# Optimization experiments

Measured on AMD Instinct MI355X. Metric: run time of the kernel, lower is better.

## Reference

```python
import jax, jax.numpy as jnp
import numpy as np

DIM = 1024
H = 8
HK = DIM // H  # head key dim = 128 (expand_k=1.0)
HV = DIM // H  # head value dim = 128 (expand_v=1.0)
GLR = 16       # gate low-rank dim (fla default)
GATE_LOGIT_NORMALIZER = 16.0
EPS = 1e-5
B, T = 2, 512


def setup_inputs() -> dict:
    key = jax.random.key(0)
    ks = jax.random.split(key, 9)
    s = lambda k, shp: jax.random.normal(k, shp, jnp.float32) * (shp[0] ** -0.5)
    return {
        "x": jax.random.normal(ks[0], (B, T, DIM), jnp.float32),
        "Wq": s(ks[1], (DIM, DIM)),
        "Wk": s(ks[2], (DIM, DIM)),
        "Wv": s(ks[3], (DIM, DIM)),
        "Wg": s(ks[4], (DIM, DIM)),
        "Wgk1": s(ks[5], (DIM, GLR)),
        "Wgk2": s(ks[6], (GLR, DIM)),
        "bgk2": jnp.zeros((DIM,), jnp.float32),
        "g_norm_w": jnp.ones((HV,), jnp.float32),
        "Wo": s(ks[7], (DIM, DIM)),
    }


def _gla_forward(x, Wq, Wk, Wv, Wg, Wgk1, Wgk2, bgk2, g_norm_w, Wo):
    b, t, _ = x.shape
    # projections
    q = (x @ Wq).reshape(b, t, H, HK) * (HK ** -0.5)
    k = (x @ Wk).reshape(b, t, H, HK)
    v = (x @ Wv).reshape(b, t, H, HV)
    # low-rank forget gate: logsigmoid / normalizer, per key channel
    gk = (jax.nn.log_sigmoid((x @ Wgk1) @ Wgk2 + bgk2) / GATE_LOGIT_NORMALIZER)
    gk = gk.reshape(b, t, H, HK)

    # recurrent decay-gated linear attention:
    #   S_t = diag(exp(gk_t)) @ S_{t-1} + k_t^T v_t ; o_t = q_t @ S_t
    def step(h, inp):
        qt, kt, vt, gt = inp  # each [B, H, HK] / [B, H, HV]
        h = h * jnp.exp(gt)[..., None] + kt[..., None] * vt[..., None, :]
        ot = jnp.einsum("bhk,bhkv->bhv", qt, h)
        return h, ot

    h0 = jnp.zeros((b, H, HK, HV), x.dtype)
    xs = (
        q.transpose(1, 0, 2, 3),
        k.transpose(1, 0, 2, 3),
        v.transpose(1, 0, 2, 3),
        gk.transpose(1, 0, 2, 3),
    )
    _, o = jax.lax.scan(step, h0, xs)  # o: [T, B, H, HV]
    o = o.transpose(1, 0, 2, 3)        # [B, T, H, HV]

    # gated RMSNorm with swish gate over per-head value dim, then output proj
    g = (x @ Wg).reshape(b, t, H, HV)
    rms = jax.lax.rsqrt(jnp.mean(o * o, axis=-1, keepdims=True) + EPS)
    o = (o * rms) * g_norm_w * (g * jax.nn.sigmoid(g))
    return o.reshape(b, t, DIM) @ Wo


def reference(x, Wq, Wk, Wv, Wg, Wgk1, Wgk2, bgk2, g_norm_w, Wo):
    return _gla_forward(x, Wq, Wk, Wv, Wg, Wgk1, Wgk2, bgk2, g_norm_w, Wo)
```

## Files before the change

kernel.cpp:

```cpp
#include <hip/hip_runtime.h>
#include <hip/hip_bf16.h>
#include <math.h>

#define BT     1024
#define NH     8
#define SEGLEN 32
#define NSEG   16
#define NBH    16
#define QKS    136
#define VTS    40
#define AMS    40

typedef __attribute__((ext_vector_type(8))) short short8;
typedef __attribute__((ext_vector_type(4))) short sh4;
typedef __attribute__((ext_vector_type(4))) float f32x4;

__device__ __forceinline__ float bitf(short u) {
    union { float f; unsigned i; } x; x.i = ((unsigned)(unsigned short)u) << 16; return x.f;
}
__device__ __forceinline__ short f2bf(float f) {
    union { float f; unsigned u; } x; x.f = f;
    unsigned r = x.u + 0x7FFF + ((x.u >> 16) & 1);
    return (short)(r >> 16);
}
__device__ __forceinline__ void gload_lds16(const short* g, short* l) {
    __builtin_amdgcn_global_load_lds(
        (const __attribute__((address_space(1))) unsigned int*)g,
        (__attribute__((address_space(3))) unsigned int*)l, 16, 0, 0);
}

__global__ __launch_bounds__(256) void cast_all(
    const float* __restrict__ Wq, const float* __restrict__ Wk,
    const float* __restrict__ Wv, const float* __restrict__ Wg,
    const float* __restrict__ Wo, const float* __restrict__ X,
    short* __restrict__ WT, short* __restrict__ Xb)
{
    const int z = blockIdx.z;
    const int tid = threadIdx.x;
    if (z == 5) {
        const int id = blockIdx.y * 32 + blockIdx.x;
        const int i = id * 1024 + tid * 4;
        float4 a = *(const float4*)(X + i);
        sh4 v;
        v[0] = f2bf(a.x); v[1] = f2bf(a.y); v[2] = f2bf(a.z); v[3] = f2bf(a.w);
        *(sh4*)(Xb + i) = v;
        return;
    }
    const float* W = (z == 0) ? Wq : (z == 1) ? Wk : (z == 2) ? Wv : (z == 3) ? Wg : Wo;
    short* T = WT + (size_t)z * (1u << 20);
    __shared__ float tile[32][33];
    const int k0 = blockIdx.y * 32, n0 = blockIdx.x * 32;
    const int row = tid >> 3, c4 = (tid & 7) << 2;
    float4 f = *(const float4*)(W + (size_t)(k0 + row) * 1024 + n0 + c4);
    tile[row][c4 + 0] = f.x; tile[row][c4 + 1] = f.y;
    tile[row][c4 + 2] = f.z; tile[row][c4 + 3] = f.w;
    __syncthreads();
    short* o = T + (size_t)(n0 + row) * 1024 + k0 + c4;
    o[0] = f2bf(tile[c4 + 0][row]); o[1] = f2bf(tile[c4 + 1][row]);
    o[2] = f2bf(tile[c4 + 2][row]); o[3] = f2bf(tile[c4 + 3][row]);
}

__global__ __launch_bounds__(256) void proj_gemm(
    const short* __restrict__ Xb, const short* __restrict__ WT,
    short* __restrict__ QKVG)
{
    const int z = blockIdx.z;
    const float scale = (z == 0) ? 0.08838834764831845f : 1.0f;
    short* C = QKVG + (size_t)z * (1u << 20);
    const short* B = WT + (size_t)z * (1u << 20);

    __shared__ __align__(16) short As[8 * 64 * 8];
    __shared__ __align__(16) short Bs[8 * 128 * 8];
    const int tid = threadIdx.x;
    const int wave = tid >> 6, lane = tid & 63;
    const int wm = (wave >> 1) * 32, wn = (wave & 1) * 64;
    const int m15 = lane & 15, q = lane >> 4;
    const int m0 = blockIdx.y * 64, n0 = blockIdx.x * 128;

    f32x4 acc[2][4];
    #pragma unroll
    for (int i = 0; i < 2; i++)
        #pragma unroll
        for (int j = 0; j < 4; j++)
            acc[i][j] = (f32x4){0.f, 0.f, 0.f, 0.f};

    for (int kb0 = 0; kb0 < 1024; kb0 += 64) {
        __syncthreads();
        #pragma unroll
        for (int c = 0; c < 2; c++) {
            const int k8 = wave * 2 + c;
            gload_lds16(Xb + (size_t)(m0 + lane) * 1024 + kb0 + k8 * 8,
                        &As[(k8 * 64) * 8]);
            #pragma unroll
            for (int rh = 0; rh < 2; rh++)
                gload_lds16(B + (size_t)(n0 + rh * 64 + lane) * 1024 + kb0 + k8 * 8,
                            &Bs[(k8 * 128 + rh * 64) * 8]);
        }
        __syncthreads();
        #pragma unroll
        for (int s = 0; s < 2; s++) {
            const int k8 = s * 4 + q;
            short8 af[2], bf[4];
            #pragma unroll
            for (int i = 0; i < 2; i++)
                af[i] = *(const short8*)&As[(k8 * 64 + wm + i * 16 + m15) * 8];
            #pragma unroll
            for (int j = 0; j < 4; j++)
                bf[j] = *(const short8*)&Bs[(k8 * 128 + wn + j * 16 + m15) * 8];
            #pragma unroll
            for (int i = 0; i < 2; i++)
                #pragma unroll
                for (int j = 0; j < 4; j++)
                    acc[i][j] = __builtin_amdgcn_mfma_f32_16x16x32_bf16(af[i], bf[j], acc[i][j], 0, 0, 0);
        }
    }
    #pragma unroll
    for (int i = 0; i < 2; i++)
        #pragma unroll
        for (int j = 0; j < 4; j++)
            #pragma unroll
            for (int rr = 0; rr < 4; rr++)
                C[(size_t)(m0 + wm + i * 16 + q * 4 + rr) * 1024 + n0 + wn + j * 16 + m15] =
                    f2bf(acc[i][j][rr] * scale);
}

__global__ __launch_bounds__(256) void wo_gemm(
    const short* __restrict__ A, const short* __restrict__ B, float* __restrict__ C)
{
    __shared__ __align__(16) short As[8 * 64 * 8];
    __shared__ __align__(16) short Bs[8 * 64 * 8];
    const int tid = threadIdx.x;
    const int wave = tid >> 6, lane = tid & 63;
    const int wm = (wave >> 1) * 32, wn = (wave & 1) * 32;
    const int m15 = lane & 15, q = lane >> 4;
    const int m0 = blockIdx.y * 64, n0 = blockIdx.x * 64;

    f32x4 acc[2][2];
    #pragma unroll
    for (int i = 0; i < 2; i++)
        #pragma unroll
        for (int j = 0; j < 2; j++)
            acc[i][j] = (f32x4){0.f, 0.f, 0.f, 0.f};

    for (int kb0 = 0; kb0 < 1024; kb0 += 64) {
        __syncthreads();
        #pragma unroll
        for (int c = 0; c < 2; c++) {
            const int k8 = wave * 2 + c;
            gload_lds16(A + (size_t)(m0 + lane) * 1024 + kb0 + k8 * 8, &As[(k8 * 64) * 8]);
            gload_lds16(B + (size_t)(n0 + lane) * 1024 + kb0 + k8 * 8, &Bs[(k8 * 64) * 8]);
        }
        __syncthreads();
        #pragma unroll
        for (int s = 0; s < 2; s++) {
            const int k8 = s * 4 + q;
            short8 af[2], bf[2];
            #pragma unroll
            for (int i = 0; i < 2; i++)
                af[i] = *(const short8*)&As[(k8 * 64 + wm + i * 16 + m15) * 8];
            #pragma unroll
            for (int j = 0; j < 2; j++)
                bf[j] = *(const short8*)&Bs[(k8 * 64 + wn + j * 16 + m15) * 8];
            #pragma unroll
            for (int i = 0; i < 2; i++)
                #pragma unroll
                for (int j = 0; j < 2; j++)
                    acc[i][j] = __builtin_amdgcn_mfma_f32_16x16x32_bf16(af[i], bf[j], acc[i][j], 0, 0, 0);
        }
    }
    #pragma unroll
    for (int i = 0; i < 2; i++)
        #pragma unroll
        for (int j = 0; j < 2; j++)
            #pragma unroll
            for (int rr = 0; rr < 4; rr++)
                C[(size_t)(m0 + wm + i * 16 + q * 4 + rr) * 1024 + n0 + wn + j * 16 + m15] =
                    acc[i][j][rr];
}

__global__ __launch_bounds__(256) void gk_proj(
    const short* __restrict__ Xb, const float* __restrict__ Wgk1,
    const float* __restrict__ Wgk2, const float* __restrict__ bgk2,
    short* __restrict__ GK)
{
    const int row = blockIdx.x, tid = threadIdx.x;
    float p[16];
    #pragma unroll
    for (int j = 0; j < 16; j++) p[j] = 0.f;
    for (int d = tid; d < 1024; d += 256) {
        float xv = bitf(Xb[(size_t)row * 1024 + d]);
        #pragma unroll
        for (int j = 0; j < 16; j++)
            p[j] = fmaf(xv, Wgk1[d * 16 + j], p[j]);
    }
    #pragma unroll
    for (int j = 0; j < 16; j++)
        for (int off = 32; off; off >>= 1) p[j] += __shfl_down(p[j], off);
    __shared__ float zp[4][16];
    __shared__ float z[16];
    const int lane = tid & 63, w = tid >> 6;
    if (lane == 0) {
        #pragma unroll
        for (int j = 0; j < 16; j++) zp[w][j] = p[j];
    }
    __syncthreads();
    if (tid < 16) z[tid] = zp[0][tid] + zp[1][tid] + zp[2][tid] + zp[3][tid];
    __syncthreads();
    for (int c = tid; c < 1024; c += 256) {
        float acc = bgk2[c];
        #pragma unroll
        for (int j = 0; j < 16; j++)
            acc = fmaf(z[j], Wgk2[j * 1024 + c], acc);
        float ls = fminf(acc, 0.f) - log1pf(expf(-fabsf(acc)));
        GK[(size_t)row * 1024 + c] = f2bf(ls * (1.f / 16.f));
    }
}

__global__ __launch_bounds__(256) void scan_chunk(
    const short* __restrict__ Q, const short* __restrict__ K,
    const short* __restrict__ V, short* GKQT,
    float* __restrict__ O, short* __restrict__ SS, float* __restrict__ DSEG)
{
    const int seg = blockIdx.x;
    const int bh  = blockIdx.y;
    const int b = bh >> 3, h = bh & 7;
    const int tid = threadIdx.x;
    const size_t rowbase = (size_t)(b * 512 + seg * SEGLEN) * 1024 + h * 128;

    __shared__ __align__(16) short Qt[32 * QKS];
    __shared__ __align__(16) short Kt[32 * QKS];
    __shared__ __align__(16) short Vs[32 * 128];
    __shared__ __align__(16) short VT[128 * VTS];
    __shared__ __align__(16) short KhT[128 * VTS];
    __shared__ __align__(16) short Am[32 * AMS];

    if (tid < 128) {
        const int ch = tid;
        float gsum = 0.f;
        float ktf[32];
        #pragma unroll
        for (int t = 0; t < 32; t++) {
            const size_t a = rowbase + (size_t)t * 1024 + ch;
            float g  = bitf(GKQT[a]);
            float kv = bitf(K[a]);
            float qv = bitf(Q[a]);
            gsum += g;
            float eg  = expf(gsum);
            float emg = expf(-gsum);
            short qts = f2bf(qv * eg);
            Qt[t * QKS + ch] = qts;
            GKQT[a] = qts;
            float ktv = kv * emg;
            Kt[t * QKS + ch] = f2bf(ktv);
            ktf[t] = ktv;
        }
        float eGend = expf(gsum);
        DSEG[(bh * NSEG + seg) * 128 + ch] = eGend;
        #pragma unroll
        for (int t4 = 0; t4 < 8; t4++) {
            sh4 p;
            p[0] = f2bf(ktf[4 * t4 + 0] * eGend);
            p[1] = f2bf(ktf[4 * t4 + 1] * eGend);
            p[2] = f2bf(ktf[4 * t4 + 2] * eGend);
            p[3] = f2bf(ktf[4 * t4 + 3] * eGend);
            *(sh4*)&KhT[ch * VTS + 4 * t4] = p;
        }
    } else {
        const int u = tid - 128;
        #pragma unroll
        for (int i = 0; i < 4; i++) {
            const int idx = u + i * 128;
            const int t = idx >> 4, c = idx & 15;
            short8 vv = *(const short8*)&V[rowbase + (size_t)t * 1024 + c * 8];
            *(short8*)&Vs[t * 128 + c * 8] = vv;
        }
    }
    __syncthreads();
    {
        const int ch = tid >> 1, t0 = (tid & 1) * 16;
        #pragma unroll
        for (int j = 0; j < 4; j++) {
            sh4 p;
            p[0] = Vs[(t0 + 4 * j + 0) * 128 + ch];
            p[1] = Vs[(t0 + 4 * j + 1) * 128 + ch];
            p[2] = Vs[(t0 + 4 * j + 2) * 128 + ch];
            p[3] = Vs[(t0 + 4 * j + 3) * 128 + ch];
            *(sh4*)&VT[ch * VTS + t0 + 4 * j] = p;
        }
    }
    __syncthreads();

    const int wave = tid >> 6, lane = tid & 63;
    const int m15 = lane & 15, q = lane >> 4;

    {
        const int mi = wave >> 1, ni = wave & 1;
        f32x4 a1 = (f32x4){0.f, 0.f, 0.f, 0.f};
        #pragma unroll
        for (int kc = 0; kc < 4; kc++) {
            short8 af = *(const short8*)&Qt[(mi * 16 + m15) * QKS + kc * 32 + q * 8];
            short8 bf = *(const short8*)&Kt[(ni * 16 + m15) * QKS + kc * 32 + q * 8];
            a1 = __builtin_amdgcn_mfma_f32_16x16x32_bf16(af, bf, a1, 0, 0, 0);
        }
        #pragma unroll
        for (int rr = 0; rr < 4; rr++) {
            const int t = mi * 16 + q * 4 + rr, s = ni * 16 + m15;
            Am[t * AMS + s] = (t >= s) ? f2bf(a1[rr]) : (short)0;
        }
    }
    __syncthreads();

    {
        const int mi = wave >> 1, nb = (wave & 1) * 4;
        short8 af = *(const short8*)&Am[(mi * 16 + m15) * AMS + q * 8];
        #pragma unroll
        for (int jj = 0; jj < 4; jj++) {
            short8 bf = *(const short8*)&VT[((nb + jj) * 16 + m15) * VTS + q * 8];
            f32x4 a2 = (f32x4){0.f, 0.f, 0.f, 0.f};
            a2 = __builtin_amdgcn_mfma_f32_16x16x32_bf16(af, bf, a2, 0, 0, 0);
            #pragma unroll
            for (int rr = 0; rr < 4; rr++)
                O[rowbase + (size_t)(mi * 16 + q * 4 + rr) * 1024 + (nb + jj) * 16 + m15] = a2[rr];
        }
    }

    {
        const size_t sbase = (size_t)(bh * NSEG + seg) * 16384;
        #pragma unroll
        for (int m2 = 0; m2 < 2; m2++) {
            const int mrow = wave * 2 + m2;
            short8 af = *(const short8*)&KhT[(mrow * 16 + m15) * VTS + q * 8];
            #pragma unroll
            for (int ni = 0; ni < 8; ni++) {
                short8 bf = *(const short8*)&VT[(ni * 16 + m15) * VTS + q * 8];
                f32x4 a3 = (f32x4){0.f, 0.f, 0.f, 0.f};
                a3 = __builtin_amdgcn_mfma_f32_16x16x32_bf16(af, bf, a3, 0, 0, 0);
                #pragma unroll
                for (int rr = 0; rr < 4; rr++)
                    SS[sbase + (size_t)(mrow * 16 + q * 4 + rr) * 128 + ni * 16 + m15] =
                        f2bf(a3[rr]);
            }
        }
    }
}

__global__ __launch_bounds__(256) void stitch(
    short* __restrict__ SS, const float* __restrict__ DSEG)
{
    const int slice = blockIdx.x;
    const int bh = blockIdx.y, tid = threadIdx.x;
    __shared__ float dloc[NSEG][16];
    dloc[tid >> 4][tid & 15] = DSEG[(bh * NSEG + (tid >> 4)) * 128 + slice * 16 + (tid & 15)];
    __syncthreads();
    float run[8];
    #pragma unroll
    for (int j = 0; j < 8; j++) run[j] = 0.f;
    for (int seg = 0; seg < NSEG; seg++) {
        const size_t base = (size_t)(bh * NSEG + seg) * 16384 + slice * 2048;
        #pragma unroll
        for (int j = 0; j < 8; j++) {
            const int e = j * 256 + tid;
            float tmp = bitf(SS[base + e]);
            SS[base + e] = f2bf(run[j]);
            run[j] = fmaf(run[j], dloc[seg][(e >> 7)], tmp);
        }
    }
}

__global__ __launch_bounds__(256) void corr_gnorm(
    const short* __restrict__ QT, const short* __restrict__ SS,
    const float* __restrict__ O, const short* __restrict__ G,
    const float* __restrict__ gnw, short* __restrict__ Obf)
{
    const int seg = blockIdx.x;
    const int bh = blockIdx.y;
    const int b = bh >> 3, h = bh & 7;
    const int tid = threadIdx.x;
    __shared__ float qt[SEGLEN][128];
    __shared__ float red[4][16];
    const size_t rowbase = (size_t)(b * 512 + seg * SEGLEN) * 1024 + h * 128;
    {
        const int t = tid >> 3, c0 = (tid & 7) * 16;
        #pragma unroll
        for (int c = 0; c < 16; c++)
            qt[t][c0 + c] = bitf(QT[rowbase + (size_t)t * 1024 + c0 + c]);
    }
    __syncthreads();
    const size_t sbase = (size_t)(bh * NSEG + seg) * 16384;
    const int v = tid & 127, th = tid >> 7;
    float acc[16];
    #pragma unroll
    for (int tt = 0; tt < 16; tt++) acc[tt] = 0.f;
    for (int k = 0; k < 128; k++) {
        float sv = bitf(SS[sbase + (size_t)k * 128 + v]);
        #pragma unroll
        for (int tt = 0; tt < 16; tt++)
            acc[tt] = fmaf(qt[th * 16 + tt][k], sv, acc[tt]);
    }
    float o[16], ss[16];
    #pragma unroll
    for (int tt = 0; tt < 16; tt++) {
        const int t = th * 16 + tt;
        o[tt] = O[rowbase + (size_t)t * 1024 + v] + acc[tt];
        ss[tt] = o[tt] * o[tt];
    }
    #pragma unroll
    for (int tt = 0; tt < 16; tt++)
        #pragma unroll
        for (int off = 32; off; off >>= 1)
            ss[tt] += __shfl_xor(ss[tt], off);
    const int wv = tid >> 6;
    if ((tid & 63) == 0) {
        #pragma unroll
        for (int tt = 0; tt < 16; tt++) red[wv][tt] = ss[tt];
    }
    __syncthreads();
    const float gw = gnw[v];
    #pragma unroll
    for (int tt = 0; tt < 16; tt++) {
        const int t = th * 16 + tt;
        float ms = (red[th * 2][tt] + red[th * 2 + 1][tt]) * (1.f / 128.f);
        float r = rsqrtf(ms + 1e-5f);
        float g = bitf(G[rowbase + (size_t)t * 1024 + v]);
        float sg = g / (1.f + expf(-g));
        Obf[rowbase + (size_t)t * 1024 + v] = f2bf(o[tt] * r * gw * sg);
    }
}

extern "C" void kernel_launch(void* const* d_in, const int* in_sizes, int n_in,
                              void* d_out, int out_size, void* d_ws, size_t ws_size,
                              hipStream_t stream)
{
    const float* X    = (const float*)d_in[0];
    const float* Wq   = (const float*)d_in[1];
    const float* Wk   = (const float*)d_in[2];
    const float* Wv   = (const float*)d_in[3];
    const float* Wg   = (const float*)d_in[4];
    const float* Wgk1 = (const float*)d_in[5];
    const float* Wgk2 = (const float*)d_in[6];
    const float* bgk2 = (const float*)d_in[7];
    const float* gnw  = (const float*)d_in[8];
    const float* Wo   = (const float*)d_in[9];
    float* OUT = (float*)d_out;

    short* QKVG = (short*)d_ws;
    short* GK   = QKVG + (4u << 20);
    float* Ob   = (float*)(GK + (1u << 20));
    short* SS   = (short*)(Ob + (1u << 20));
    float* DS   = (float*)(SS + (4u << 20));
    short* WT   = (short*)(DS + 32768);
    short* Xb   = WT + (5u << 20);
    short* Obf  = QKVG;

    cast_all<<<dim3(32, 32, 6), 256, 0, stream>>>(Wq, Wk, Wv, Wg, Wo, X, WT, Xb);
    proj_gemm<<<dim3(8, 16, 4), 256, 0, stream>>>(Xb, WT, QKVG);
    gk_proj<<<dim3(BT), 256, 0, stream>>>(Xb, Wgk1, Wgk2, bgk2, GK);
    scan_chunk<<<dim3(NSEG, NBH), 256, 0, stream>>>(
        QKVG, QKVG + (1u << 20), QKVG + (2u << 20), GK, Ob, SS, DS);
    stitch<<<dim3(8, NBH), 256, 0, stream>>>(SS, DS);
    corr_gnorm<<<dim3(NSEG, NBH), 256, 0, stream>>>(
        GK, SS, Ob, QKVG + (3u << 20), gnw, Obf);
    wo_gemm<<<dim3(16, 16), 256, 0, stream>>>(Obf, WT + (4u << 20), OUT);
}
```

Measured before the change: 174.1 us.

## Use MFMA for inter-chunk correction, transpose state layout, shrink proj tiles

The chunk state in SS is now stored transposed (value-major), and the stitch kernel is changed to match, so each thread now uses a single per-key decay value. corr_gnorm replaces its scalar FMA loop over the 128-wide state with bf16 MFMA tiles loaded into LDS asynchronously, and does the RMS reduction with lane shuffles within 16-lane groups. proj_gemm tiles drop from 64x128 to 64x64 and the grid doubles, which gives more blocks and better occupancy but less reuse of each loaded tile.

```diff
diff --git a/kernel.cpp b/kernel.cpp
--- a/kernel.cpp
+++ b/kernel.cpp
@@ -70,18 +70,18 @@
     const short* B = WT + (size_t)z * (1u << 20);
 
     __shared__ __align__(16) short As[8 * 64 * 8];
-    __shared__ __align__(16) short Bs[8 * 128 * 8];
+    __shared__ __align__(16) short Bs[8 * 64 * 8];
     const int tid = threadIdx.x;
     const int wave = tid >> 6, lane = tid & 63;
-    const int wm = (wave >> 1) * 32, wn = (wave & 1) * 64;
+    const int wm = (wave >> 1) * 32, wn = (wave & 1) * 32;
     const int m15 = lane & 15, q = lane >> 4;
-    const int m0 = blockIdx.y * 64, n0 = blockIdx.x * 128;
-
-    f32x4 acc[2][4];
+    const int m0 = blockIdx.y * 64, n0 = blockIdx.x * 64;
+
+    f32x4 acc[2][2];
     #pragma unroll
     for (int i = 0; i < 2; i++)
         #pragma unroll
-        for (int j = 0; j < 4; j++)
+        for (int j = 0; j < 2; j++)
             acc[i][j] = (f32x4){0.f, 0.f, 0.f, 0.f};
 
     for (int kb0 = 0; kb0 < 1024; kb0 += 64) {
@@ -89,35 +89,31 @@
         #pragma unroll
         for (int c = 0; c < 2; c++) {
             const int k8 = wave * 2 + c;
-            gload_lds16(Xb + (size_t)(m0 + lane) * 1024 + kb0 + k8 * 8,
-                        &As[(k8 * 64) * 8]);
-            #pragma unroll
-            for (int rh = 0; rh < 2; rh++)
-                gload_lds16(B + (size_t)(n0 + rh * 64 + lane) * 1024 + kb0 + k8 * 8,
-                            &Bs[(k8 * 128 + rh * 64) * 8]);
+            gload_lds16(Xb + (size_t)(m0 + lane) * 1024 + kb0 + k8 * 8, &As[(k8 * 64) * 8]);
+            gload_lds16(B  + (size_t)(n0 + lane) * 1024 + kb0 + k8 * 8, &Bs[(k8 * 64) * 8]);
         }
         __syncthreads();
         #pragma unroll
         for (int s = 0; s < 2; s++) {
             const int k8 = s * 4 + q;
-            short8 af[2], bf[4];
+            short8 af[2], bf[2];
             #pragma unroll
             for (int i = 0; i < 2; i++)
                 af[i] = *(const short8*)&As[(k8 * 64 + wm + i * 16 + m15) * 8];
             #pragma unroll
-            for (int j = 0; j < 4; j++)
-                bf[j] = *(const short8*)&Bs[(k8 * 128 + wn + j * 16 + m15) * 8];
+            for (int j = 0; j < 2; j++)
+                bf[j] = *(const short8*)&Bs[(k8 * 64 + wn + j * 16 + m15) * 8];
             #pragma unroll
             for (int i = 0; i < 2; i++)
                 #pragma unroll
-                for (int j = 0; j < 4; j++)
+                for (int j = 0; j < 2; j++)
                     acc[i][j] = __builtin_amdgcn_mfma_f32_16x16x32_bf16(af[i], bf[j], acc[i][j], 0, 0, 0);
         }
     }
     #pragma unroll
     for (int i = 0; i < 2; i++)
         #pragma unroll
-        for (int j = 0; j < 4; j++)
+        for (int j = 0; j < 2; j++)
             #pragma unroll
             for (int rr = 0; rr < 4; rr++)
                 C[(size_t)(m0 + wm + i * 16 + q * 4 + rr) * 1024 + n0 + wn + j * 16 + m15] =
@@ -329,10 +325,10 @@
         #pragma unroll
         for (int m2 = 0; m2 < 2; m2++) {
             const int mrow = wave * 2 + m2;
-            short8 af = *(const short8*)&KhT[(mrow * 16 + m15) * VTS + q * 8];
+            short8 af = *(const short8*)&VT[(mrow * 16 + m15) * VTS + q * 8];
             #pragma unroll
             for (int ni = 0; ni < 8; ni++) {
-                short8 bf = *(const short8*)&VT[(ni * 16 + m15) * VTS + q * 8];
+                short8 bf = *(const short8*)&KhT[(ni * 16 + m15) * VTS + q * 8];
                 f32x4 a3 = (f32x4){0.f, 0.f, 0.f, 0.f};
                 a3 = __builtin_amdgcn_mfma_f32_16x16x32_bf16(af, bf, a3, 0, 0, 0);
                 #pragma unroll
@@ -349,20 +345,23 @@
 {
     const int slice = blockIdx.x;
     const int bh = blockIdx.y, tid = threadIdx.x;
-    __shared__ float dloc[NSEG][16];
-    dloc[tid >> 4][tid & 15] = DSEG[(bh * NSEG + (tid >> 4)) * 128 + slice * 16 + (tid & 15)];
-    __syncthreads();
+    __shared__ float dloc[NSEG][128];
+    for (int i = tid; i < NSEG * 128; i += 256)
+        dloc[i >> 7][i & 127] = DSEG[(bh * NSEG + (i >> 7)) * 128 + (i & 127)];
+    __syncthreads();
+    const int kch = tid & 127;
     float run[8];
     #pragma unroll
     for (int j = 0; j < 8; j++) run[j] = 0.f;
     for (int seg = 0; seg < NSEG; seg++) {
         const size_t base = (size_t)(bh * NSEG + seg) * 16384 + slice * 2048;
+        const float dk = dloc[seg][kch];
         #pragma unroll
         for (int j = 0; j < 8; j++) {
             const int e = j * 256 + tid;
             float tmp = bitf(SS[base + e]);
             SS[base + e] = f2bf(run[j]);
-            run[j] = fmaf(run[j], dloc[seg][(e >> 7)], tmp);
+            run[j] = fmaf(run[j], dk, tmp);
         }
     }
 }
@@ -376,54 +375,87 @@
     const int bh = blockIdx.y;
     const int b = bh >> 3, h = bh & 7;
     const int tid = threadIdx.x;
-    __shared__ float qt[SEGLEN][128];
+    const int wave = tid >> 6, lane = tid & 63;
+    const int m15 = lane & 15, q = lane >> 4;
+    const size_t rowbase = (size_t)(b * 512 + seg * SEGLEN) * 1024 + h * 128;
+    const size_t sbase = (size_t)(bh * NSEG + seg) * 16384;
+
+    __shared__ __align__(16) short Qs[16 * 32 * 8];
+    __shared__ __align__(16) short Ss[16 * 128 * 8];
     __shared__ float red[4][16];
-    const size_t rowbase = (size_t)(b * 512 + seg * SEGLEN) * 1024 + h * 128;
-    {
-        const int t = tid >> 3, c0 = (tid & 7) * 16;
-        #pragma unroll
-        for (int c = 0; c < 16; c++)
-            qt[t][c0 + c] = bitf(QT[rowbase + (size_t)t * 1024 + c0 + c]);
-    }
-    __syncthreads();
-    const size_t sbase = (size_t)(bh * NSEG + seg) * 16384;
-    const int v = tid & 127, th = tid >> 7;
-    float acc[16];
-    #pragma unroll
-    for (int tt = 0; tt < 16; tt++) acc[tt] = 0.f;
-    for (int k = 0; k < 128; k++) {
-        float sv = bitf(SS[sbase + (size_t)k * 128 + v]);
-        #pragma unroll
-        for (int tt = 0; tt < 16; tt++)
-            acc[tt] = fmaf(qt[th * 16 + tt][k], sv, acc[tt]);
-    }
-    float o[16], ss[16];
-    #pragma unroll
-    for (int tt = 0; tt < 16; tt++) {
-        const int t = th * 16 + tt;
-        o[tt] = O[rowbase + (size_t)t * 1024 + v] + acc[tt];
-        ss[tt] = o[tt] * o[tt];
-    }
-    #pragma unroll
-    for (int tt = 0; tt < 16; tt++)
-        #pragma unroll
-        for (int off = 32; off; off >>= 1)
-            ss[tt] += __shfl_xor(ss[tt], off);
-    const int wv = tid >> 6;
-    if ((tid & 63) == 0) {
-        #pragma unroll
-        for (int tt = 0; tt < 16; tt++) red[wv][tt] = ss[tt];
-    }
-    __syncthreads();
-    const float gw = gnw[v];
-    #pragma unroll
-    for (int tt = 0; tt < 16; tt++) {
-        const int t = th * 16 + tt;
-        float ms = (red[th * 2][tt] + red[th * 2 + 1][tt]) * (1.f / 128.f);
-        float r = rsqrtf(ms + 1e-5f);
-        float g = bitf(G[rowbase + (size_t)t * 1024 + v]);
-        float sg = g / (1.f + expf(-g));
-        Obf[rowbase + (size_t)t * 1024 + v] = f2bf(o[tt] * r * gw * sg);
+
+    #pragma unroll
+    for (int c = 0; c < 2; c++) {
+        const int fb = wave * 128 + c * 64;
+        const int flat = fb + lane;
+        const int k8 = flat >> 5, t = flat & 31;
+        gload_lds16(QT + rowbase + (size_t)t * 1024 + k8 * 8, &Qs[fb * 8]);
+    }
+    #pragma unroll
+    for (int c = 0; c < 8; c++) {
+        const int fb = wave * 512 + c * 64;
+        const int flat = fb + lane;
+        const int k8 = flat >> 7, vch = flat & 127;
+        gload_lds16(SS + sbase + (size_t)vch * 128 + k8 * 8, &Ss[fb * 8]);
+    }
+    __syncthreads();
+
+    const int mt = wave >> 1, nh2 = wave & 1;
+    f32x4 acc[4];
+    #pragma unroll
+    for (int nt = 0; nt < 4; nt++) acc[nt] = (f32x4){0.f, 0.f, 0.f, 0.f};
+    #pragma unroll
+    for (int kb = 0; kb < 4; kb++) {
+        short8 af = *(const short8*)&Qs[((kb * 4 + q) * 32 + mt * 16 + m15) * 8];
+        #pragma unroll
+        for (int nt = 0; nt < 4; nt++) {
+            short8 bf = *(const short8*)&Ss[((kb * 4 + q) * 128 + nh2 * 64 + nt * 16 + m15) * 8];
+            acc[nt] = __builtin_amdgcn_mfma_f32_16x16x32_bf16(af, bf, acc[nt], 0, 0, 0);
+        }
+    }
+
+    float o[4][4];
+    float ssq[4] = {0.f, 0.f, 0.f, 0.f};
+    #pragma unroll
+    for (int nt = 0; nt < 4; nt++) {
+        const int vch = nh2 * 64 + nt * 16 + m15;
+        #pragma unroll
+        for (int rr = 0; rr < 4; rr++) {
+            const int t = mt * 16 + q * 4 + rr;
+            float ov = O[rowbase + (size_t)t * 1024 + vch] + acc[nt][rr];
+            o[nt][rr] = ov;
+            ssq[rr] = fmaf(ov, ov, ssq[rr]);
+        }
+    }
+    #pragma unroll
+    for (int rr = 0; rr < 4; rr++) {
+        ssq[rr] += __shfl_xor(ssq[rr], 1);
+        ssq[rr] += __shfl_xor(ssq[rr], 2);
+        ssq[rr] += __shfl_xor(ssq[rr], 4);
+        ssq[rr] += __shfl_xor(ssq[rr], 8);
+    }
+    if (m15 == 0) {
+        #pragma unroll
+        for (int rr = 0; rr < 4; rr++) red[wave][q * 4 + rr] = ssq[rr];
+    }
+    __syncthreads();
+    float rsq[4];
+    #pragma unroll
+    for (int rr = 0; rr < 4; rr++) {
+        float ms = (red[wave][q * 4 + rr] + red[wave ^ 1][q * 4 + rr]) * (1.f / 128.f);
+        rsq[rr] = rsqrtf(ms + 1e-5f);
+    }
+    #pragma unroll
+    for (int nt = 0; nt < 4; nt++) {
+        const int vch = nh2 * 64 + nt * 16 + m15;
+        const float gw = gnw[vch];
+        #pragma unroll
+        for (int rr = 0; rr < 4; rr++) {
+            const int t = mt * 16 + q * 4 + rr;
+            float g = bitf(G[rowbase + (size_t)t * 1024 + vch]);
+            float sg = g / (1.f + expf(-g));
+            Obf[rowbase + (size_t)t * 1024 + vch] = f2bf(o[nt][rr] * rsq[rr] * gw * sg);
+        }
     }
 }
 
@@ -453,7 +485,7 @@
     short* Obf  = QKVG;
 
     cast_all<<<dim3(32, 32, 6), 256, 0, stream>>>(Wq, Wk, Wv, Wg, Wo, X, WT, Xb);
-    proj_gemm<<<dim3(8, 16, 4), 256, 0, stream>>>(Xb, WT, QKVG);
+    proj_gemm<<<dim3(16, 16, 4), 256, 0, stream>>>(Xb, WT, QKVG);
     gk_proj<<<dim3(BT), 256, 0, stream>>>(Xb, Wgk1, Wgk2, bgk2, GK);
     scan_chunk<<<dim3(NSEG, NBH), 256, 0, stream>>>(
         QKVG, QKVG + (1u << 20), QKVG + (2u << 20), GK, Ob, SS, DS);
```

Result: no change. 175.3 us (+0.7%).
